# Kernel tuning notes

Measured on AMD Instinct MI355X. Metric: run time of the kernel, lower is better.

## Reference

```python
import jax, jax.numpy as jnp
import numpy as np

N = 100000   # nodes
E = 1000000  # edges
G = 64       # graphs in batch
DIN, DH, DOUT = 128, 128, 64
BN_EPS = 1e-5


def setup_inputs() -> dict:
    key = jax.random.key(0)
    ks = jax.random.split(key, 20)
    inp = {}
    inp['x'] = jax.random.normal(ks[0], (N, DIN), dtype=jnp.float32)
    inp['edge_index'] = jax.random.randint(ks[1], (2, E), 0, N, dtype=jnp.int64)
    inp['batch'] = jnp.sort(jax.random.randint(ks[2], (N,), 0, G, dtype=jnp.int64))
    # GCN conv weights (stored [in, out]) + biases
    s = lambda k, i, o: jax.random.normal(k, (i, o), dtype=jnp.float32) / np.sqrt(i)
    inp['W1'] = s(ks[3], DIN, DH);  inp['b1'] = jnp.zeros((DH,), jnp.float32)
    inp['W2'] = s(ks[4], DH, DH);   inp['b2'] = jnp.zeros((DH,), jnp.float32)
    inp['W3'] = s(ks[5], DH, DOUT); inp['b3'] = jnp.zeros((DOUT,), jnp.float32)
    # BatchNorm params/buffers (eval mode)
    inp['g1'] = jnp.ones((DH,), jnp.float32);  inp['beta1'] = jnp.zeros((DH,), jnp.float32)
    inp['g2'] = jnp.ones((DH,), jnp.float32);  inp['beta2'] = jnp.zeros((DH,), jnp.float32)
    inp['mean1'] = jnp.zeros((DH,), jnp.float32); inp['var1'] = jnp.ones((DH,), jnp.float32)
    inp['mean2'] = jnp.zeros((DH,), jnp.float32); inp['var2'] = jnp.ones((DH,), jnp.float32)
    # GlobalAttention gate_nn: Linear(DOUT,DH) ReLU Linear(DH,1)
    inp['Wg1'] = s(ks[6], DOUT, DH); inp['bg1'] = jnp.zeros((DH,), jnp.float32)
    inp['Wg2'] = s(ks[7], DH, 1);    inp['bg2'] = jnp.zeros((1,), jnp.float32)
    # head MLP: Linear(DOUT,DH) ReLU Linear(DH,DOUT)
    inp['Wm1'] = s(ks[8], DOUT, DH); inp['bm1'] = jnp.zeros((DH,), jnp.float32)
    inp['Wm2'] = s(ks[9], DH, DOUT); inp['bm2'] = jnp.zeros((DOUT,), jnp.float32)
    return inp


def _gcn_conv(x, W, b, src, dst):
    # PyG GCNConv: add self-loops, sym-normalize, linear, scatter-sum, bias
    h = x @ W                                            # [N, out]
    deg = jnp.ones((N,), h.dtype).at[dst].add(1.0)       # in-degree + self-loop
    dinv = jax.lax.rsqrt(deg)
    norm = dinv[src] * dinv[dst]                         # [E]
    msg = h[src] * norm[:, None]                         # gather + scale
    out = jax.ops.segment_sum(msg, dst, num_segments=N)  # scatter
    out = out + h * (dinv * dinv)[:, None]               # self-loop term
    return out + b


def _bn(x, g, beta, mean, var):
    return (x - mean) * jax.lax.rsqrt(var + BN_EPS) * g + beta


def reference(x, edge_index, batch, W1, b1, W2, b2, W3, b3,
              g1, beta1, g2, beta2, mean1, var1, mean2, var2,
              Wg1, bg1, Wg2, bg2, Wm1, bm1, Wm2, bm2):
    src, dst = edge_index[0], edge_index[1]
    h = jax.nn.relu(_bn(_gcn_conv(x, W1, b1, src, dst), g1, beta1, mean1, var1))
    h = jax.nn.relu(_bn(_gcn_conv(h, W2, b2, src, dst), g2, beta2, mean2, var2))
    h = _gcn_conv(h, W3, b3, src, dst)                   # [N, DOUT]
    # GlobalAttention pooling: per-graph softmax of gate scores
    gate = jax.nn.relu(h @ Wg1 + bg1) @ Wg2 + bg2        # [N, 1]
    gate = gate[:, 0]
    m = jax.ops.segment_max(gate, batch, num_segments=G)
    e = jnp.exp(gate - m[batch])
    s = jax.ops.segment_sum(e, batch, num_segments=G)
    a = e / s[batch]                                     # [N]
    pooled = jax.ops.segment_sum(h * a[:, None], batch, num_segments=G)  # [G, DOUT]
    # MLP head (dropout off in eval)
    return jax.nn.relu(pooled @ Wm1 + bm1) @ Wm2 + bm2   # [G, DOUT]
```

## Files before the change

### kernel.cpp

```cpp
#include <hip/hip_runtime.h>
#include <hip/hip_bf16.h>
#include <hip/hip_fp16.h>
#include <math.h>

#define NN 100000
#define EE 1000000
#define GG 64
#define BN_EPS 1e-5f
#define CPB 16
#define EB 4096
#define NBLK ((EE + EB - 1) / EB)
#define NBUCK ((NN + 511) / 512)

typedef __attribute__((ext_vector_type(8))) short bf16x8;
typedef __attribute__((ext_vector_type(4))) float f32x4;

__device__ inline short f2bf(float f) {
  unsigned u = __float_as_uint(f);
  u = u + 0x7fff + ((u >> 16) & 1);
  return (short)(u >> 16);
}
__device__ inline float bf2f(short h) {
  return __uint_as_float(((unsigned)(unsigned short)h) << 16);
}

__device__ inline unsigned fenc(float f) {
  int b = __float_as_int(f);
  return (b < 0) ? ~(unsigned)b : ((unsigned)b | 0x80000000u);
}
__device__ inline float fdec(unsigned u) {
  int b = (u & 0x80000000u) ? (int)(u & 0x7fffffffu) : (int)~u;
  return __int_as_float(b);
}

__device__ inline void acc2(float& a0, float& a1, unsigned u) {
  asm("v_fma_mix_f32 %0, %2, 1.0, %0 op_sel:[0,0,0] op_sel_hi:[1,0,0]\n\t"
      "v_fma_mix_f32 %1, %2, 1.0, %1 op_sel:[1,0,0] op_sel_hi:[1,0,0]"
      : "+v"(a0), "+v"(a1)
      : "v"(u));
}
__device__ inline void acc8(float* a, uint4 u) {
  acc2(a[0], a[1], u.x);
  acc2(a[2], a[3], u.y);
  acc2(a[4], a[5], u.z);
  acc2(a[6], a[7], u.w);
}
__device__ inline uint4 zsel(uint4 u, int ok) {
  uint4 r;
  r.x = ok ? u.x : 0u;
  r.y = ok ? u.y : 0u;
  r.z = ok ? u.z : 0u;
  r.w = ok ? u.w : 0u;
  return r;
}

__global__ __launch_bounds__(256) void k_bhist(const int* __restrict__ dst,
                                               int* __restrict__ bhist, int E) {
  __shared__ int h[256];
  int t = threadIdx.x;
  h[t] = 0;
  __syncthreads();
  int base = blockIdx.x * EB;
#pragma unroll
  for (int j = 0; j < EB / 256; ++j) {
    int i = base + j * 256 + t;
    if (i < E) atomicAdd(&h[dst[i] >> 9], 1);
  }
  __syncthreads();
  bhist[blockIdx.x * 256 + t] = h[t];
}

__global__ __launch_bounds__(256) void k_bscan1(int* __restrict__ bhist,
                                                int* __restrict__ btot) {
  __shared__ int s[256];
  int bin = blockIdx.x, t = threadIdx.x;
  int v = (t < NBLK) ? bhist[t * 256 + bin] : 0;
  s[t] = v;
  __syncthreads();
  for (int o = 1; o < 256; o <<= 1) {
    int u = (t >= o) ? s[t - o] : 0;
    __syncthreads();
    s[t] += u;
    __syncthreads();
  }
  if (t < NBLK) bhist[t * 256 + bin] = s[t] - v;
  if (t == 255) btot[bin] = s[255];
}

__global__ __launch_bounds__(256) void k_bscan2(const int* __restrict__ btot,
                                                int* __restrict__ bstart) {
  __shared__ int s[256];
  int t = threadIdx.x;
  int v = btot[t];
  s[t] = v;
  __syncthreads();
  for (int o = 1; o < 256; o <<= 1) {
    int u = (t >= o) ? s[t - o] : 0;
    __syncthreads();
    s[t] += u;
    __syncthreads();
  }
  bstart[t] = s[t] - v;
}

__global__ __launch_bounds__(256) void k_bscat(const int* __restrict__ src,
                                               const int* __restrict__ dst,
                                               const int* __restrict__ bhist,
                                               const int* __restrict__ bstart,
                                               int2* __restrict__ pairs, int E) {
  __shared__ int h[256];
  __shared__ int base[256];
  int t = threadIdx.x;
  h[t] = 0;
  __syncthreads();
  int b0 = blockIdx.x * EB;
  int ds[EB / 256], rk[EB / 256];
#pragma unroll
  for (int j = 0; j < EB / 256; ++j) {
    int i = b0 + j * 256 + t;
    if (i < E) {
      int d = dst[i];
      ds[j] = d;
      rk[j] = atomicAdd(&h[d >> 9], 1);
    } else
      ds[j] = -1;
  }
  __syncthreads();
  base[t] = bstart[t] + bhist[blockIdx.x * 256 + t];
  __syncthreads();
#pragma unroll
  for (int j = 0; j < EB / 256; ++j) {
    int i = b0 + j * 256 + t;
    if (ds[j] >= 0) {
      int pos = base[ds[j] >> 9] + rk[j];
      pairs[pos] = make_int2(src[i], ds[j]);
    }
  }
}

__global__ __launch_bounds__(256) void k_bfill(const int2* __restrict__ pairs,
                                               const int* __restrict__ bstart,
                                               int* __restrict__ rowstart,
                                               int* __restrict__ eidx,
                                               float* __restrict__ dinv, int N,
                                               int E) {
  __shared__ int h[512];
  __shared__ int ex[512];
  __shared__ int ps[256];
  const int b = blockIdx.x;
  const int n0 = b << 9;
  const int e0 = bstart[b], e1 = bstart[b + 1];
  const int t = threadIdx.x;
  h[t] = 0;
  h[t + 256] = 0;
  __syncthreads();
  for (int i = e0 + t; i < e1; i += 256) atomicAdd(&h[pairs[i].y - n0], 1);
  __syncthreads();
  int v0 = h[2 * t], v1 = h[2 * t + 1];
  int sp = v0 + v1;
  ps[t] = sp;
  __syncthreads();
  for (int o = 1; o < 256; o <<= 1) {
    int u = (t >= o) ? ps[t - o] : 0;
    __syncthreads();
    ps[t] += u;
    __syncthreads();
  }
  int ex0 = ps[t] - sp;
  ex[2 * t] = ex0;
  ex[2 * t + 1] = ex0 + v0;
  __syncthreads();
  for (int i = t; i < 512; i += 256) {
    int node = n0 + i;
    if (node < N) {
      rowstart[node] = e0 + ex[i];
      dinv[node] = rsqrtf(1.0f + (float)h[i]);
    }
  }
  if (b == 0 && t == 0) rowstart[N] = E;
  __syncthreads();
  for (int i = e0 + t; i < e1; i += 256) {
    int2 p = pairs[i];
    int r = atomicAdd(&ex[p.y - n0], 1);
    eidx[e0 + r] = p.x;
  }
}

__global__ __launch_bounds__(256) void k_wsplit(const float* __restrict__ W1,
                                                const float* __restrict__ W2,
                                                const float* __restrict__ W3,
                                                const float* __restrict__ Wg1,
                                                short* __restrict__ wt) {
  int i = blockIdx.x * 256 + threadIdx.x;
  const float* W;
  short *hi, *lo;
  int K, M, idx;
  if (i < 16384) {
    W = W1; hi = wt; lo = wt + 16384; K = 128; M = 128; idx = i;
  } else if (i < 32768) {
    W = W2; hi = wt + 32768; lo = wt + 49152; K = 128; M = 128; idx = i - 16384;
  } else if (i < 40960) {
    W = W3; hi = wt + 65536; lo = wt + 73728; K = 128; M = 64; idx = i - 32768;
  } else {
    W = Wg1; hi = wt + 81920; lo = wt + 90112; K = 64; M = 128; idx = i - 40960;
  }
  int k = idx / M, n = idx % M;
  float w = W[idx];
  short h = f2bf(w);
  hi[n * K + k] = h;
  lo[n * K + k] = f2bf(w - bf2f(h));
}

__global__ __launch_bounds__(256) void k_bnprep(
    const float* __restrict__ g1, const float* __restrict__ b1,
    const float* __restrict__ m1, const float* __restrict__ v1,
    const float* __restrict__ g2, const float* __restrict__ b2,
    const float* __restrict__ m2, const float* __restrict__ v2,
    float* __restrict__ s1, float* __restrict__ h1, float* __restrict__ s2,
    float* __restrict__ h2) {
  int i = threadIdx.x;
  if (i < 128) {
    float s = g1[i] * rsqrtf(v1[i] + BN_EPS);
    s1[i] = s;
    h1[i] = b1[i] - m1[i] * s;
  } else {
    int j = i - 128;
    float s = g2[j] * rsqrtf(v2[j] + BN_EPS);
    s2[j] = s;
    h2[j] = b2[j] - m2[j] * s;
  }
}

template <int K, int M, int AIN, int DINV, int GATE, int OUTH>
__global__ __launch_bounds__(256, 2) void k_mgemm(
    const float* __restrict__ Xf, const short* __restrict__ Xhi,
    const short* __restrict__ Xlo, const short* __restrict__ Wthi,
    const short* __restrict__ Wtlo, const float* __restrict__ dinv,
    const float* __restrict__ gbias, const float* __restrict__ Wg2v,
    const float* __restrict__ bg2v, void* __restrict__ Y,
    float* __restrict__ gate, int nrows) {
  constexpr int NC = K / 32;
  constexpr int CT = M / 16;
  constexpr int R = 2;
  const int lane = threadIdx.x & 63;
  const int wave = threadIdx.x >> 6;
  const int m16 = lane & 15;
  const int quad = lane >> 4;
  const int rowbase = blockIdx.x * 128 + wave * 32;

  bf16x8 ahi[R][NC], alo[R][NC];
#pragma unroll
  for (int t = 0; t < R; ++t) {
    const int arow = rowbase + t * 16 + m16;
    const bool rok = arow < nrows;
#pragma unroll
    for (int c = 0; c < NC; ++c) {
      const int k0 = c * 32 + quad * 8;
      if constexpr (AIN) {
        if (rok) {
          ahi[t][c] = *(const bf16x8*)(Xhi + (size_t)arow * K + k0);
          alo[t][c] = *(const bf16x8*)(Xlo + (size_t)arow * K + k0);
        } else {
          ahi[t][c] = bf16x8{0, 0, 0, 0, 0, 0, 0, 0};
          alo[t][c] = bf16x8{0, 0, 0, 0, 0, 0, 0, 0};
        }
      } else {
        float4 v0 = make_float4(0.f, 0.f, 0.f, 0.f), v1 = v0;
        if (rok) {
          v0 = *(const float4*)(Xf + (size_t)arow * K + k0);
          v1 = *(const float4*)(Xf + (size_t)arow * K + k0 + 4);
        }
        float vv[8] = {v0.x, v0.y, v0.z, v0.w, v1.x, v1.y, v1.z, v1.w};
#pragma unroll
        for (int j = 0; j < 8; ++j) {
          short h = f2bf(vv[j]);
          ahi[t][c][j] = h;
          alo[t][c][j] = f2bf(vv[j] - bf2f(h));
        }
      }
    }
  }

  float dv[R][4];
  if constexpr (DINV && !GATE) {
#pragma unroll
    for (int t = 0; t < R; ++t)
#pragma unroll
      for (int r = 0; r < 4; ++r) {
        int row = rowbase + t * 16 + quad * 4 + r;
        dv[t][r] = (row < nrows) ? dinv[row] : 0.f;
      }
  }

  float gp[R][4];
  if constexpr (GATE) {
#pragma unroll
    for (int t = 0; t < R; ++t)
#pragma unroll
      for (int r = 0; r < 4; ++r) gp[t][r] = 0.f;
  }

#pragma unroll
  for (int ct = 0; ct < CT; ++ct) {
    bf16x8 bhi[NC], blo[NC];
    const size_t wrow = (size_t)(ct * 16 + m16) * K + quad * 8;
#pragma unroll
    for (int c = 0; c < NC; ++c) {
      bhi[c] = *(const bf16x8*)(Wthi + wrow + c * 32);
      blo[c] = *(const bf16x8*)(Wtlo + wrow + c * 32);
    }
#pragma unroll
    for (int t = 0; t < R; ++t) {
      f32x4 acc = {0.f, 0.f, 0.f, 0.f};
#pragma unroll
      for (int c = 0; c < NC; ++c) {
        acc = __builtin_amdgcn_mfma_f32_16x16x32_bf16(ahi[t][c], bhi[c], acc, 0, 0, 0);
        acc = __builtin_amdgcn_mfma_f32_16x16x32_bf16(ahi[t][c], blo[c], acc, 0, 0, 0);
        acc = __builtin_amdgcn_mfma_f32_16x16x32_bf16(alo[t][c], bhi[c], acc, 0, 0, 0);
      }
      if constexpr (GATE) {
        const int col = ct * 16 + m16;
        const float gb = gbias[col], wg = Wg2v[col];
#pragma unroll
        for (int r = 0; r < 4; ++r) gp[t][r] += fmaxf(acc[r] + gb, 0.f) * wg;
      } else {
#pragma unroll
        for (int r = 0; r < 4; ++r) {
          const int row = rowbase + t * 16 + quad * 4 + r;
          if (row < nrows) {
            float v = acc[r];
            if constexpr (DINV) v *= dv[t][r];
            if constexpr (OUTH)
              ((__half*)Y)[(size_t)row * M + ct * 16 + m16] = __float2half(v);
            else
              ((float*)Y)[(size_t)row * M + ct * 16 + m16] = v;
          }
        }
      }
    }
  }
  if constexpr (GATE) {
#pragma unroll
    for (int o = 1; o < 16; o <<= 1) {
#pragma unroll
      for (int t = 0; t < R; ++t)
#pragma unroll
        for (int r = 0; r < 4; ++r) gp[t][r] += __shfl_xor(gp[t][r], o, 64);
    }
    if (m16 == 0) {
      const float b2 = bg2v[0];
#pragma unroll
      for (int t = 0; t < R; ++t)
#pragma unroll
        for (int r = 0; r < 4; ++r) {
          const int row = rowbase + t * 16 + quad * 4 + r;
          if (row < nrows) gate[row] = gp[t][r] + b2;
        }
    }
  }
}

template <int M, int EPI>
__global__ __launch_bounds__(256) void k_agg(const __half* __restrict__ hp,
                                             const int* __restrict__ rowstart,
                                             const int* __restrict__ eidx,
                                             const float* __restrict__ dinv,
                                             const float* __restrict__ bias,
                                             const float* __restrict__ bns,
                                             const float* __restrict__ bnh,
                                             float* __restrict__ outf,
                                             short* __restrict__ ohi,
                                             short* __restrict__ olo, int N) {
  constexpr int LPR = M / 8;
  constexpr int NPW = 64 / (2 * LPR);
  const int wv = (blockIdx.x * 256 + threadIdx.x) >> 6;
  const int lane = threadIdx.x & 63;
  const int grp = lane / (2 * LPR);
  const int slot = (lane / LPR) & 1;
  const int sub = lane % LPR;
  const int w = wv * NPW + grp;
  if (w >= N) return;
  const unsigned subo = (unsigned)sub * 16u;
  const float di = dinv[w];
  const int lo = rowstart[w], hi = rowstart[w + 1];
  const int hi1 = hi - 1;
  const char* hpb = (const char*)hp;
  float a[8] = {0.f, 0.f, 0.f, 0.f, 0.f, 0.f, 0.f, 0.f};

  int e = lo + slot;
  while (e < hi) {
    int idx[8], ss[8];
    uint4 uu[8];
#pragma unroll
    for (int p = 0; p < 8; ++p) {
      idx[p] = e + 2 * p;
      ss[p] = eidx[min(idx[p], hi1)];
    }
#pragma unroll
    for (int p = 0; p < 8; ++p)
      uu[p] = *(const uint4*)(hpb + ((unsigned)ss[p] * (unsigned)(M * 2) + subo));
#pragma unroll
    for (int p = 0; p < 8; ++p) {
      uu[p] = zsel(uu[p], idx[p] < hi);
      acc8(a, uu[p]);
    }
    e += 16;
  }
#pragma unroll
  for (int j = 0; j < 8; ++j) a[j] += __shfl_xor(a[j], LPR, 64);

  if (slot != 0) return;
  uint4 us = *(const uint4*)(hpb + ((unsigned)w * (unsigned)(M * 2) + subo));
  acc8(a, us);
  float4 b0 = *(const float4*)(bias + sub * 8);
  float4 b1 = *(const float4*)(bias + sub * 8 + 4);
  float r[8];
  r[0] = a[0] * di + b0.x;
  r[1] = a[1] * di + b0.y;
  r[2] = a[2] * di + b0.z;
  r[3] = a[3] * di + b0.w;
  r[4] = a[4] * di + b1.x;
  r[5] = a[5] * di + b1.y;
  r[6] = a[6] * di + b1.z;
  r[7] = a[7] * di + b1.w;
  if constexpr (EPI) {
    float4 s0 = *(const float4*)(bns + sub * 8);
    float4 s1 = *(const float4*)(bns + sub * 8 + 4);
    float4 h0 = *(const float4*)(bnh + sub * 8);
    float4 h1 = *(const float4*)(bnh + sub * 8 + 4);
    float sv[8] = {s0.x, s0.y, s0.z, s0.w, s1.x, s1.y, s1.z, s1.w};
    float hv[8] = {h0.x, h0.y, h0.z, h0.w, h1.x, h1.y, h1.z, h1.w};
    short hs[8], ls[8];
#pragma unroll
    for (int j = 0; j < 8; ++j) {
      float ev = fmaxf(r[j] * sv[j] + hv[j], 0.f);
      short hb = f2bf(ev);
      float res = ev - bf2f(hb);
      hs[j] = hb;
      ls[j] = (short)(__float_as_uint(res) >> 16);
    }
    *(short4*)(ohi + (size_t)w * M + sub * 8) = make_short4(hs[0], hs[1], hs[2], hs[3]);
    *(short4*)(ohi + (size_t)w * M + sub * 8 + 4) = make_short4(hs[4], hs[5], hs[6], hs[7]);
    *(short4*)(olo + (size_t)w * M + sub * 8) = make_short4(ls[0], ls[1], ls[2], ls[3]);
    *(short4*)(olo + (size_t)w * M + sub * 8 + 4) = make_short4(ls[4], ls[5], ls[6], ls[7]);
  } else {
    *(float4*)(outf + (size_t)w * M + sub * 8) = make_float4(r[0], r[1], r[2], r[3]);
    *(float4*)(outf + (size_t)w * M + sub * 8 + 4) = make_float4(r[4], r[5], r[6], r[7]);
  }
}

__global__ __launch_bounds__(128) void k_gbounds(const int* __restrict__ batch,
                                                 int* __restrict__ gstart,
                                                 int N) {
  int g = threadIdx.x;
  if (g > GG) return;
  int lo = 0, hi = N;
  while (lo < hi) {
    int mid = (lo + hi) >> 1;
    if (batch[mid] < g) lo = mid + 1;
    else hi = mid;
  }
  gstart[g] = lo;
}

__global__ __launch_bounds__(256) void k_pmax(const float* __restrict__ gate,
                                              const int* __restrict__ gstart,
                                              unsigned* __restrict__ gmaxu) {
  __shared__ unsigned red[256];
  const int g = blockIdx.x / CPB;
  const int c = blockIdx.x % CPB;
  const int lo = gstart[g], hi = gstart[g + 1];
  const int len = hi - lo;
  const int b0 = lo + (int)(((long long)len * c) / CPB);
  const int b1 = lo + (int)(((long long)len * (c + 1)) / CPB);
  unsigned mx = 0u;
  for (int i = b0 + threadIdx.x; i < b1; i += 256) mx = max(mx, fenc(gate[i]));
  red[threadIdx.x] = mx;
  __syncthreads();
  for (int o = 128; o; o >>= 1) {
    if (threadIdx.x < o)
      red[threadIdx.x] = max(red[threadIdx.x], red[threadIdx.x + o]);
    __syncthreads();
  }
  if (threadIdx.x == 0 && red[0] != 0u) atomicMax(&gmaxu[g], red[0]);
}

__global__ __launch_bounds__(256) void k_psum(const float* __restrict__ gate,
                                              const float* __restrict__ h3,
                                              const unsigned* __restrict__ gmaxu,
                                              const int* __restrict__ gstart,
                                              float* __restrict__ pooledw,
                                              float* __restrict__ ssum) {
  __shared__ float accs[4][64];
  __shared__ float ses[4];
  const int g = blockIdx.x / CPB;
  const int c = blockIdx.x % CPB;
  const int lo = gstart[g], hi = gstart[g + 1];
  const int len = hi - lo;
  const int b0 = lo + (int)(((long long)len * c) / CPB);
  const int b1 = lo + (int)(((long long)len * (c + 1)) / CPB);
  const int wave = threadIdx.x >> 6, lane = threadIdx.x & 63;
  const float m = fdec(gmaxu[g]);
  float acc = 0.f, se = 0.f;
  for (int i = b0 + wave; i < b1; i += 4) {
    float e = expf(gate[i] - m);
    acc += e * h3[(size_t)i * 64 + lane];
    se += e;
  }
  accs[wave][lane] = acc;
  if (lane == 0) ses[wave] = se;
  __syncthreads();
  if (threadIdx.x < 64) {
    float a = accs[0][threadIdx.x] + accs[1][threadIdx.x] +
              accs[2][threadIdx.x] + accs[3][threadIdx.x];
    if (a != 0.f) atomicAdd(&pooledw[g * 64 + threadIdx.x], a);
  }
  if (threadIdx.x == 64) {
    float s = ses[0] + ses[1] + ses[2] + ses[3];
    if (s != 0.f) atomicAdd(&ssum[g], s);
  }
}

__global__ __launch_bounds__(256) void k_head(const float* __restrict__ pooledw,
                                              const float* __restrict__ ssum,
                                              const float* __restrict__ Wm1,
                                              const float* __restrict__ bm1,
                                              const float* __restrict__ Wm2,
                                              const float* __restrict__ bm2,
                                              float* __restrict__ out) {
  __shared__ float P[64 * 64];
  __shared__ float T[64 * 128];
  int tid = threadIdx.x;
  for (int i = tid; i < 4096; i += 256) {
    float s = ssum[i >> 6];
    P[i] = pooledw[i] * ((s > 0.f) ? 1.0f / s : 0.f);
  }
  __syncthreads();
  for (int e = tid; e < 8192; e += 256) {
    int r = e >> 7, c = e & 127;
    float a = bm1[c];
    for (int k = 0; k < 64; ++k) a += P[r * 64 + k] * Wm1[k * 128 + c];
    T[e] = fmaxf(a, 0.f);
  }
  __syncthreads();
  for (int e = tid; e < 4096; e += 256) {
    int r = e >> 6, c = e & 63;
    float a = bm2[c];
    for (int k = 0; k < 128; ++k) a += T[r * 128 + k] * Wm2[k * 64 + c];
    out[e] = a;
  }
}

extern "C" void kernel_launch(void* const* d_in, const int* in_sizes, int n_in,
                              void* d_out, int out_size, void* d_ws,
                              size_t ws_size, hipStream_t stream) {
  const int N = NN, E = EE;
  const float* x = (const float*)d_in[0];
  const int* ei = (const int*)d_in[1];
  const int* batch = (const int*)d_in[2];
  const float* W1 = (const float*)d_in[3];
  const float* b1 = (const float*)d_in[4];
  const float* W2 = (const float*)d_in[5];
  const float* b2 = (const float*)d_in[6];
  const float* W3 = (const float*)d_in[7];
  const float* b3 = (const float*)d_in[8];
  const float* g1 = (const float*)d_in[9];
  const float* beta1 = (const float*)d_in[10];
  const float* g2 = (const float*)d_in[11];
  const float* beta2 = (const float*)d_in[12];
  const float* mean1 = (const float*)d_in[13];
  const float* var1 = (const float*)d_in[14];
  const float* mean2 = (const float*)d_in[15];
  const float* var2 = (const float*)d_in[16];
  const float* Wg1 = (const float*)d_in[17];
  const float* bg1 = (const float*)d_in[18];
  const float* Wg2 = (const float*)d_in[19];
  const float* bg2 = (const float*)d_in[20];
  const float* Wm1 = (const float*)d_in[21];
  const float* bm1 = (const float*)d_in[22];
  const float* Wm2 = (const float*)d_in[23];
  const float* bm2 = (const float*)d_in[24];
  float* out = (float*)d_out;

  const int* src = ei;
  const int* dst = ei + E;

  char* wsb = (char*)d_ws;
  size_t off = 0;
  auto alloc = [&](size_t elems) -> void* {
    void* p = wsb + off;
    off += elems * 4;
    return p;
  };
  int* rowstart = (int*)alloc(N + 4);
  int* eidx = (int*)alloc(E);
  int2* pairs = (int2*)alloc((size_t)E * 2);
  int* bhist = (int*)alloc(NBLK * 256 + 256);
  int* btot = (int*)alloc(256);
  int* bstart = (int*)alloc(256);
  float* dinv = (float*)alloc(N);
  float* gate = (float*)alloc(N);
  __half* hbuf = (__half*)alloc((size_t)N * 64);
  short* ahi_p = (short*)alloc((size_t)N * 64);
  short* alo_p = (short*)alloc((size_t)N * 64);
  float* fbuf = (float*)alloc((size_t)N * 64);
  short* wt = (short*)alloc(49152);
  float* bn1s = (float*)alloc(128);
  float* bn1h = (float*)alloc(128);
  float* bn2s = (float*)alloc(128);
  float* bn2h = (float*)alloc(128);
  float* pooledw = (float*)alloc(GG * 64);
  float* ssum = (float*)alloc(GG);
  unsigned* gmaxu = (unsigned*)alloc(GG);
  int* gstart = (int*)alloc(GG + 4);
  (void)ws_size;
  (void)n_in;
  (void)in_sizes;
  (void)out_size;

  hipMemsetAsync(pooledw, 0, (GG * 64 + GG + GG) * sizeof(float), stream);
  k_bhist<<<NBLK, 256, 0, stream>>>(dst, bhist, E);
  k_bscan1<<<256, 256, 0, stream>>>(bhist, btot);
  k_bscan2<<<1, 256, 0, stream>>>(btot, bstart);
  k_bscat<<<NBLK, 256, 0, stream>>>(src, dst, bhist, bstart, pairs, E);
  k_bfill<<<NBUCK, 256, 0, stream>>>(pairs, bstart, rowstart, eidx, dinv, N, E);

  k_wsplit<<<192, 256, 0, stream>>>(W1, W2, W3, Wg1, wt);
  k_bnprep<<<1, 256, 0, stream>>>(g1, beta1, mean1, var1, g2, beta2, mean2,
                                  var2, bn1s, bn1h, bn2s, bn2h);
  k_gbounds<<<1, 128, 0, stream>>>(batch, gstart, N);

  const int gbb = (N + 127) / 128;
  const int ab128 = (N + 7) / 8;
  const int ab64 = (N + 15) / 16;

  k_mgemm<128, 128, 0, 1, 0, 1><<<gbb, 256, 0, stream>>>(
      x, nullptr, nullptr, wt, wt + 16384, dinv, nullptr, nullptr, nullptr,
      hbuf, nullptr, N);
  k_agg<128, 1><<<ab128, 256, 0, stream>>>(hbuf, rowstart, eidx, dinv, b1,
                                           bn1s, bn1h, nullptr, ahi_p, alo_p,
                                           N);

  k_mgemm<128, 128, 1, 1, 0, 1><<<gbb, 256, 0, stream>>>(
      nullptr, ahi_p, alo_p, wt + 32768, wt + 49152, dinv, nullptr, nullptr,
      nullptr, hbuf, nullptr, N);
  k_agg<128, 1><<<ab128, 256, 0, stream>>>(hbuf, rowstart, eidx, dinv, b2,
                                           bn2s, bn2h, nullptr, ahi_p, alo_p,
                                           N);

  k_mgemm<128, 64, 1, 1, 0, 1><<<gbb, 256, 0, stream>>>(
      nullptr, ahi_p, alo_p, wt + 65536, wt + 73728, dinv, nullptr, nullptr,
      nullptr, hbuf, nullptr, N);
  k_agg<64, 0><<<ab64, 256, 0, stream>>>(hbuf, rowstart, eidx, dinv, b3,
                                         nullptr, nullptr, fbuf, nullptr,
                                         nullptr, N);

  k_mgemm<64, 128, 0, 0, 1, 0><<<gbb, 256, 0, stream>>>(
      fbuf, nullptr, nullptr, wt + 81920, wt + 90112, nullptr, bg1, Wg2, bg2,
      nullptr, gate, N);

  k_pmax<<<GG * CPB, 256, 0, stream>>>(gate, gstart, gmaxu);
  k_psum<<<GG * CPB, 256, 0, stream>>>(gate, fbuf, gmaxu, gstart, pooledw,
                                       ssum);

  k_head<<<1, 256, 0, stream>>>(pooledw, ssum, Wm1, bm1, Wm2, bm2, out);
}
```

Measured before the change: 513.8 us.

## Stage GEMM weights in LDS and split output columns across a 2D grid

```diff
diff --git a/kernel.cpp b/kernel.cpp
--- a/kernel.cpp
+++ b/kernel.cpp
@@ -231,8 +231,8 @@
   }
 }
 
-template <int K, int M, int AIN, int DINV, int GATE, int OUTH>
-__global__ __launch_bounds__(256, 2) void k_mgemm(
+template <int K, int M, int CTB, int AIN, int DINV, int GATE, int OUTH>
+__global__ __launch_bounds__(256, 3) void k_mgemm(
     const float* __restrict__ Xf, const short* __restrict__ Xhi,
     const short* __restrict__ Xlo, const short* __restrict__ Wthi,
     const short* __restrict__ Wtlo, const float* __restrict__ dinv,
@@ -240,13 +240,15 @@
     const float* __restrict__ bg2v, void* __restrict__ Y,
     float* __restrict__ gate, int nrows) {
   constexpr int NC = K / 32;
-  constexpr int CT = M / 16;
+  constexpr int KP = K + 8;
   constexpr int R = 2;
+  __shared__ short lds[2 * CTB * 16 * KP];
   const int lane = threadIdx.x & 63;
   const int wave = threadIdx.x >> 6;
   const int m16 = lane & 15;
   const int quad = lane >> 4;
   const int rowbase = blockIdx.x * 128 + wave * 32;
+  const int cbase = blockIdx.y * CTB * 16;
 
   bf16x8 ahi[R][NC], alo[R][NC];
 #pragma unroll
@@ -281,6 +283,18 @@
     }
   }
 
+  {
+    constexpr int ELEMS = CTB * 16 * K;
+#pragma unroll
+    for (int i = threadIdx.x * 8; i < ELEMS; i += 256 * 8) {
+      const int r = i / K, c = i % K;
+      *(bf16x8*)(&lds[r * KP + c]) =
+          *(const bf16x8*)(Wthi + (size_t)(cbase + r) * K + c);
+      *(bf16x8*)(&lds[CTB * 16 * KP + r * KP + c]) =
+          *(const bf16x8*)(Wtlo + (size_t)(cbase + r) * K + c);
+    }
+  }
+
   float dv[R][4];
   if constexpr (DINV && !GATE) {
 #pragma unroll
@@ -300,14 +314,16 @@
       for (int r = 0; r < 4; ++r) gp[t][r] = 0.f;
   }
 
-#pragma unroll
-  for (int ct = 0; ct < CT; ++ct) {
+  __syncthreads();
+
+#pragma unroll
+  for (int ct = 0; ct < CTB; ++ct) {
     bf16x8 bhi[NC], blo[NC];
-    const size_t wrow = (size_t)(ct * 16 + m16) * K + quad * 8;
+    const int wrow = (ct * 16 + m16) * KP + quad * 8;
 #pragma unroll
     for (int c = 0; c < NC; ++c) {
-      bhi[c] = *(const bf16x8*)(Wthi + wrow + c * 32);
-      blo[c] = *(const bf16x8*)(Wtlo + wrow + c * 32);
+      bhi[c] = *(const bf16x8*)(&lds[wrow + c * 32]);
+      blo[c] = *(const bf16x8*)(&lds[CTB * 16 * KP + wrow + c * 32]);
     }
 #pragma unroll
     for (int t = 0; t < R; ++t) {
@@ -319,7 +335,7 @@
         acc = __builtin_amdgcn_mfma_f32_16x16x32_bf16(alo[t][c], bhi[c], acc, 0, 0, 0);
       }
       if constexpr (GATE) {
-        const int col = ct * 16 + m16;
+        const int col = cbase + ct * 16 + m16;
         const float gb = gbias[col], wg = Wg2v[col];
 #pragma unroll
         for (int r = 0; r < 4; ++r) gp[t][r] += fmaxf(acc[r] + gb, 0.f) * wg;
@@ -331,9 +347,10 @@
             float v = acc[r];
             if constexpr (DINV) v *= dv[t][r];
             if constexpr (OUTH)
-              ((__half*)Y)[(size_t)row * M + ct * 16 + m16] = __float2half(v);
+              ((__half*)Y)[(size_t)row * M + cbase + ct * 16 + m16] =
+                  __float2half(v);
             else
-              ((float*)Y)[(size_t)row * M + ct * 16 + m16] = v;
+              ((float*)Y)[(size_t)row * M + cbase + ct * 16 + m16] = v;
           }
         }
       }
@@ -634,28 +651,28 @@
   const int ab128 = (N + 7) / 8;
   const int ab64 = (N + 15) / 16;
 
-  k_mgemm<128, 128, 0, 1, 0, 1><<<gbb, 256, 0, stream>>>(
+  k_mgemm<128, 128, 4, 0, 1, 0, 1><<<dim3(gbb, 2), 256, 0, stream>>>(
       x, nullptr, nullptr, wt, wt + 16384, dinv, nullptr, nullptr, nullptr,
       hbuf, nullptr, N);
   k_agg<128, 1><<<ab128, 256, 0, stream>>>(hbuf, rowstart, eidx, dinv, b1,
                                            bn1s, bn1h, nullptr, ahi_p, alo_p,
                                            N);
 
-  k_mgemm<128, 128, 1, 1, 0, 1><<<gbb, 256, 0, stream>>>(
+  k_mgemm<128, 128, 4, 1, 1, 0, 1><<<dim3(gbb, 2), 256, 0, stream>>>(
       nullptr, ahi_p, alo_p, wt + 32768, wt + 49152, dinv, nullptr, nullptr,
       nullptr, hbuf, nullptr, N);
   k_agg<128, 1><<<ab128, 256, 0, stream>>>(hbuf, rowstart, eidx, dinv, b2,
                                            bn2s, bn2h, nullptr, ahi_p, alo_p,
                                            N);
 
-  k_mgemm<128, 64, 1, 1, 0, 1><<<gbb, 256, 0, stream>>>(
+  k_mgemm<128, 64, 4, 1, 1, 0, 1><<<dim3(gbb, 1), 256, 0, stream>>>(
       nullptr, ahi_p, alo_p, wt + 65536, wt + 73728, dinv, nullptr, nullptr,
       nullptr, hbuf, nullptr, N);
   k_agg<64, 0><<<ab64, 256, 0, stream>>>(hbuf, rowstart, eidx, dinv, b3,
                                          nullptr, nullptr, fbuf, nullptr,
                                          nullptr, N);
 
-  k_mgemm<64, 128, 0, 0, 1, 0><<<gbb, 256, 0, stream>>>(
+  k_mgemm<64, 128, 8, 0, 0, 1, 0><<<dim3(gbb, 1), 256, 0, stream>>>(
       fbuf, nullptr, nullptr, wt + 81920, wt + 90112, nullptr, bg1, Wg2, bg2,
       nullptr, gate, N);
 
```

New measurement: 487.8 us. -5.1%, faster.
